# Kernel optimization log

Hardware: AMD Instinct MI355X
Metric: run time of the kernel (lower is better)

Reference implementation:

```python
import jax, jax.numpy as jnp
import numpy as np

C_IN = 96          # spectral bands
D2 = 2 * C_IN      # d = 192 (inner dim)
D4 = 4 * D2        # 768 (4-directional scan channels)
N = 16             # SSM state size
DR = 6             # delta_rank = ceil(96/16)
B, H, W = 2, 96, 96  # H,W not in {8,16,32,64} -> s=1 path


def setup_inputs() -> dict:
    key = jax.random.key(0)
    ks = jax.random.split(key, 8)
    g = lambda k, shape, s: jax.random.normal(k, shape, jnp.float32) * s
    return {
        "x": jax.random.normal(ks[0], (B, C_IN, H, W), jnp.float32),
        "W_in": g(ks[1], (C_IN, 2 * D2), 0.05),          # in_proj (in,out)
        "b_in": jnp.zeros((2 * D2,), jnp.float32),
        "w_dw": g(ks[2], (D2, 1, 3, 3), 0.1),            # depthwise conv OIHW
        "b_dw": jnp.zeros((D2,), jnp.float32),
        "A_log": jnp.log(jnp.tile(jnp.arange(1.0, N + 1.0, dtype=jnp.float32), (D4, 1))),
        "Dp": jnp.ones((D4,), jnp.float32),
        "W_x": g(ks[3], (D4, DR + 2 * N), 0.05),         # x_proj, no bias
        "W_delta": g(ks[4], (DR, D4), 0.1),
        "b_delta": g(ks[5], (D4,), 0.1),
        "ln_g": jnp.ones((D2,), jnp.float32),
        "ln_b": jnp.zeros((D2,), jnp.float32),
        "W_out": g(ks[6], (D2, C_IN), 0.05),             # out_proj, no bias
    }


def _selective_scan(u, delta, A, Bm, Cm, Dv):
    # u, delta: [b,L,d4]; Bm, Cm: [b,L,n]; A: [d4,n]; Dv: [d4]
    b, L, d4 = u.shape
    n = A.shape[1]

    def step(h, inps):
        u_t, dt, B_t, C_t = inps                      # [b,d4],[b,d4],[b,n],[b,n]
        dA = jnp.exp(dt[:, :, None] * A)              # [b,d4,n]
        h = dA * h + (dt * u_t)[:, :, None] * B_t[:, None, :]
        y = jnp.einsum('bdn,bn->bd', h, C_t) + Dv * u_t
        return h, y

    h0 = jnp.zeros((b, d4, n), u.dtype)
    xs = (jnp.swapaxes(u, 0, 1), jnp.swapaxes(delta, 0, 1),
          jnp.swapaxes(Bm, 0, 1), jnp.swapaxes(Cm, 0, 1))
    _, ys = jax.lax.scan(step, h0, xs)                # ys: [L,b,d4]
    return jnp.swapaxes(ys, 0, 1)                     # [b,L,d4]


def reference(x, W_in, b_in, w_dw, b_dw, A_log, Dp, W_x, W_delta, b_delta, ln_g, ln_b, W_out):
    b, c, Hh, Ww = x.shape                            # s = 1 (H not in {8,16,32,64})
    d = W_in.shape[1] // 2
    # in_proj on channel-last, chunk into x / gate z
    xz = jnp.einsum('bchw,ce->bhwe', x, W_in) + b_in  # [b,h,w,2d]
    xx, z = jnp.split(xz, 2, axis=-1)
    # depthwise conv + silu
    xc = jnp.transpose(xx, (0, 3, 1, 2))              # [b,d,h,w]
    xc = jax.lax.conv_general_dilated(
        xc, w_dw, (1, 1), 'SAME', feature_group_count=d,
        dimension_numbers=('NCHW', 'OIHW', 'NCHW')) + b_dw[None, :, None, None]
    xc = jax.nn.silu(xc)
    # 4 directional flattenings (with s=1: x1==x2 row-major, x3==x4 reversed)
    L = Hh * Ww
    flat = xc.reshape(b, d, L)
    flipped = xc[:, :, ::-1, ::-1].reshape(b, d, L)
    xl = jnp.swapaxes(jnp.concatenate([flat, flat, flipped, flipped], axis=1), 1, 2)  # [b,L,4d]
    # SSM parameterization
    A = -jnp.exp(A_log)                               # [4d,n]
    x_dbl = xl @ W_x                                  # [b,L,dr+2n]
    dr, n = W_delta.shape[0], A.shape[1]
    dt_r = x_dbl[..., :dr]
    Bm = x_dbl[..., dr:dr + n]
    Cm = x_dbl[..., dr + n:]
    delta = jax.nn.softplus(dt_r @ W_delta + b_delta)  # [b,L,4d]
    y = _selective_scan(xl, delta, A, Bm, Cm, Dp)      # [b,L,4d]
    # merge 4 directions back to spatial
    y = jnp.transpose(y.reshape(b, L, 4, d), (0, 2, 3, 1))  # [b,4,d,L]
    y1 = y[:, 0].reshape(b, d, Hh, Ww)
    y2 = y[:, 1].reshape(b, d, Hh, Ww)
    y3 = y[:, 2].reshape(b, d, Hh, Ww)[:, :, ::-1, ::-1]
    y4 = y[:, 3].reshape(b, d, Hh, Ww)[:, :, ::-1, ::-1]
    yh = jnp.transpose(y1 + y2 + y3 + y4, (0, 2, 3, 1))  # [b,h,w,d]
    # LayerNorm over d
    mu = yh.mean(-1, keepdims=True)
    var = ((yh - mu) ** 2).mean(-1, keepdims=True)
    yn = (yh - mu) * jax.lax.rsqrt(var + 1e-5) * ln_g + ln_b
    out = (yn * jax.nn.silu(z)) @ W_out               # [b,h,w,c]
    return jnp.transpose(out, (0, 3, 1, 2))           # [b,c,h,w]
```

## Files before the change

kernel.cpp:

```cpp
#include <hip/hip_runtime.h>
#include <hip/hip_bf16.h>
#include <math.h>

#define CIN 96
#define D2 192
#define D4 768
#define LL 9216
#define NN 16
#define NCH 288
#define CLEN 32

typedef float v2f __attribute__((ext_vector_type(2)));

#define SZ_Y4SLOT (2u*2u*9216u*192u)
#define SZ_BL    (2u*9216u*192u)
#define SZ_XDBL  (2u*9216u*38u)
#define SZ_S     (2u*4u*288u*192u)
#define SZ_HSLOT (2u*4u*288u*192u*8u)
#define F_Y4     0u
#define F_XX     0u
#define F_ZS     (F_Y4 + SZ_Y4SLOT)
#define F_XT     (F_ZS + SZ_BL)
#define F_XD0    (F_XT + SZ_BL)
#define F_XD1    (F_XD0 + SZ_XDBL)
#define F_XD2    (F_XD1 + SZ_XDBL)
#define F_XD3    (F_XD2 + SZ_XDBL)
#define F_SBUF   (F_XD3 + SZ_XDBL)
#define F_HBUF   (F_SBUF + SZ_S)
#define F_WCOMB  (F_HBUF + SZ_HSLOT)
#define F_A0     (F_WCOMB + 15360u)
#define F_FF     (F_A0 + 768u)

__device__ __forceinline__ float silu_f(float z) {
    return z / (1.0f + __expf(-z));
}

__global__ __launch_bounds__(256) void k0_foldw(
    const float* __restrict__ Wx, const float* __restrict__ Alog,
    float* __restrict__ wcomb, float* __restrict__ A0f, float* __restrict__ Ffl)
{
    int i = blockIdx.x * 256 + threadIdx.x;
    if (i < 768) {
        float a0 = -__expf(Alog[i * 16]);
        bool fast = true;
        for (int n = 1; n < 16; n++) {
            float an = -__expf(Alog[i * 16 + n]);
            float tgt = (n + 1) * a0;
            fast = fast && (fabsf(an - tgt) <= 1e-5f * fabsf(tgt));
        }
        A0f[i] = a0;
        Ffl[i] = fast ? 1.f : 0.f;
    }
    if (i >= 192 * 80) return;
    int d = i / 80, j = i % 80;
    float v = 0.f;
    if (j < 38) v = Wx[d * 38 + j] + Wx[(d + 192) * 38 + j];
    else if (j >= 40 && j < 78) {
        int jj = j - 40;
        v = Wx[(d + 384) * 38 + jj] + Wx[(d + 576) * 38 + jj];
    }
    wcomb[i] = v;
}

__global__ __launch_bounds__(256) void k1_inproj(
    const float* __restrict__ x, const float* __restrict__ Win,
    const float* __restrict__ bin, float* __restrict__ xx, float* __restrict__ zs)
{
    __shared__ float xs[96][36];
    __shared__ float wsh[96][68];
    int tid = threadIdx.x;
    int bid = blockIdx.x;
    int eh = bid & 1;
    int lt = bid >> 1;
    int gl0 = lt * 32;
    int b = gl0 / LL;
    int l0 = gl0 % LL;

    for (int i = tid; i < 96 * 32; i += 256) {
        int k = i >> 5, li = i & 31;
        xs[k][li] = x[(size_t)(b * 96 + k) * LL + l0 + li];
    }
    int lg = tid & 15;
    int eg = tid >> 4;
    for (int ch = 0; ch < 3; ch++) {
        int ecol0 = eh * 192 + ch * 64;
        __syncthreads();
        for (int i = tid; i < 96 * 64; i += 256) {
            int k = i >> 6, e = i & 63;
            wsh[k][e] = Win[k * 384 + ecol0 + e];
        }
        __syncthreads();
        v2f acc[4];
#pragma unroll
        for (int j = 0; j < 4; j++) { acc[j].x = 0.f; acc[j].y = 0.f; }
        for (int k = 0; k < 96; k++) {
            v2f x2 = *(const v2f*)&xs[k][lg * 2];
            float4 wv = *(const float4*)&wsh[k][eg * 4];
            float wa[4] = {wv.x, wv.y, wv.z, wv.w};
#pragma unroll
            for (int j = 0; j < 4; j++) {
                v2f wsp; wsp.x = wa[j]; wsp.y = wa[j];
                acc[j] += x2 * wsp;
            }
        }
        if (eh == 0) {
#pragma unroll
            for (int j = 0; j < 4; j++) {
                int e = ecol0 + eg * 4 + j;
                float bb = bin[e];
                float2 v = {acc[j].x + bb, acc[j].y + bb};
                *(float2*)&xx[(size_t)(b * 192 + e) * LL + l0 + lg * 2] = v;
            }
        } else {
            int rel0 = ch * 64 + eg * 4;
            float bb0 = bin[ecol0 + eg * 4 + 0];
            float bb1 = bin[ecol0 + eg * 4 + 1];
            float bb2 = bin[ecol0 + eg * 4 + 2];
            float bb3 = bin[ecol0 + eg * 4 + 3];
#pragma unroll
            for (int r = 0; r < 2; r++) {
                int l = l0 + lg * 2 + r;
                float4 v;
                v.x = silu_f(acc[0][r] + bb0);
                v.y = silu_f(acc[1][r] + bb1);
                v.z = silu_f(acc[2][r] + bb2);
                v.w = silu_f(acc[3][r] + bb3);
                *(float4*)&zs[((size_t)b * LL + l) * 192 + rel0] = v;
            }
        }
    }
}

__global__ __launch_bounds__(192) void k2_conv(
    const float* __restrict__ xx, const float* __restrict__ wdw,
    const float* __restrict__ bdw, float* __restrict__ xt)
{
    __shared__ float tile[32][97];
    __shared__ float wsm[32][9];
    __shared__ float bs[32];
    int tid = threadIdx.x;
    int bid = blockIdx.x;
    int h = bid % 96;
    int r = bid / 96;
    int dg = r % 6;
    int b = r / 6;

    for (int i = tid; i < 288; i += 192) wsm[i / 9][i % 9] = wdw[(dg * 32 + i / 9) * 9 + (i % 9)];
    if (tid < 32) bs[tid] = bdw[dg * 32 + tid];
    __syncthreads();

    int w = tid % 96;
    int dhalf = tid / 96;
    for (int p = 0; p < 16; p++) {
        int dsub = 2 * p + dhalf;
        const float* base = xx + (size_t)(b * 192 + dg * 32 + dsub) * LL;
        float acc = bs[dsub];
#pragma unroll
        for (int kh = 0; kh < 3; kh++) {
            int hh = h + kh - 1;
            if (hh < 0 || hh >= 96) continue;
            const float* row = base + hh * 96;
#pragma unroll
            for (int kw = 0; kw < 3; kw++) {
                int ww = w + kw - 1;
                if (ww < 0 || ww >= 96) continue;
                acc += row[ww] * wsm[dsub][kh * 3 + kw];
            }
        }
        tile[dsub][w] = silu_f(acc);
    }
    __syncthreads();
    for (int i = tid; i < 768; i += 192) {
        int q = i & 7, ls = i >> 3;
        float4 v = {tile[q * 4 + 0][ls], tile[q * 4 + 1][ls], tile[q * 4 + 2][ls], tile[q * 4 + 3][ls]};
        *(float4*)&xt[((size_t)b * LL + h * 96 + ls) * 192 + dg * 32 + q * 4] = v;
    }
}

__global__ __launch_bounds__(320) void k3_xdbl(
    const float* __restrict__ xt, const float* __restrict__ wcomb,
    float* __restrict__ xa0, float* __restrict__ xa1,
    float* __restrict__ xb0, float* __restrict__ xb1)
{
    __shared__ float xs[16][68];
    __shared__ float wsh[16][80];
    int tid = threadIdx.x;
    int bid = blockIdx.x;
    int kh = bid & 1;
    int rt = (bid >> 1) % 144;
    int b = bid / 288;
    int r0 = rt * 64;
    int k0 = kh * 96;
    float* __restrict__ xa = kh ? xa1 : xa0;
    float* __restrict__ xb = kh ? xb1 : xb0;

    int rg = tid / 20;
    int cg = tid % 20;
    v2f acc[4][2];
#pragma unroll
    for (int i = 0; i < 4; i++)
#pragma unroll
        for (int p = 0; p < 2; p++) { acc[i][p].x = 0.f; acc[i][p].y = 0.f; }

    for (int kc = 0; kc < 96; kc += 16) {
        __syncthreads();
        if (tid < 256) {
            int row = tid >> 2, dq = tid & 3;
            float4 v = *(const float4*)&xt[((size_t)b * LL + r0 + row) * 192 + k0 + kc + dq * 4];
            xs[dq * 4 + 0][row] = v.x;
            xs[dq * 4 + 1][row] = v.y;
            xs[dq * 4 + 2][row] = v.z;
            xs[dq * 4 + 3][row] = v.w;
        }
        for (int i = tid; i < 16 * 80; i += 320) {
            int d = i / 80, j = i - d * 80;
            wsh[d][j] = wcomb[(k0 + kc + d) * 80 + j];
        }
        __syncthreads();
#pragma unroll
        for (int d = 0; d < 16; d++) {
            float4 xv = *(const float4*)&xs[d][rg * 4];
            float4 wv = *(const float4*)&wsh[d][cg * 4];
            v2f w01; w01.x = wv.x; w01.y = wv.y;
            v2f w23; w23.x = wv.z; w23.y = wv.w;
            float xr[4] = {xv.x, xv.y, xv.z, xv.w};
#pragma unroll
            for (int i = 0; i < 4; i++) {
                v2f xi; xi.x = xr[i]; xi.y = xr[i];
                acc[i][0] += xi * w01;
                acc[i][1] += xi * w23;
            }
        }
    }
    int c0 = cg * 4;
#pragma unroll
    for (int i = 0; i < 4; i++) {
        int la = r0 + rg * 4 + i;
#pragma unroll
        for (int j = 0; j < 4; j++) {
            int col = c0 + j;
            float v = acc[i][j >> 1][j & 1];
            if (col < 38) {
                xa[((size_t)b * LL + la) * 38 + col] = v;
            } else if (col >= 40 && col < 78) {
                int lb = LL - 1 - la;
                xb[((size_t)b * LL + lb) * 38 + (col - 40)] = v;
            }
        }
    }
}

__global__ __launch_bounds__(192, 4) void k4_pass1(
    const float* __restrict__ xt,
    const float* __restrict__ xa0, const float* __restrict__ xa1,
    const float* __restrict__ xb0, const float* __restrict__ xb1,
    const float* __restrict__ Wd, const float* __restrict__ bdl,
    const float* __restrict__ Alog, const float* __restrict__ A0f,
    const float* __restrict__ Ffl,
    float* __restrict__ Sbuf, __hip_bfloat16* __restrict__ Hbuf)
{
    __shared__ float Bt[CLEN][16];
    __shared__ float Dt[CLEN][6];
    int tid = threadIdx.x;
    int bid = blockIdx.x;
    int k = bid % NCH;
    int r = bid / NCH;
    int dir = r & 3;
    int b = r >> 2;
    int l0 = k * CLEN;
    for (int i = tid; i < CLEN * 16; i += 192) {
        int t = i >> 4, n = i & 15;
        size_t rb = ((size_t)b * LL + l0 + t) * 38 + 6 + n;
        Bt[t][n] = (xa0[rb] + xa1[rb]) + (xb0[rb] + xb1[rb]);
    }
    for (int i = tid; i < CLEN * 6; i += 192) {
        int t = i / 6, rr = i - 6 * t;
        size_t rb = ((size_t)b * LL + l0 + t) * 38 + rr;
        Dt[t][rr] = (xa0[rb] + xa1[rb]) + (xb0[rb] + xb1[rb]);
    }
    __syncthreads();
    int c = tid;
    int d4 = dir * 192 + c;
    float a0 = A0f[d4];
    bool fast = (Ffl[d4] != 0.f);
    float wd[6];
#pragma unroll
    for (int rr = 0; rr < 6; rr++) wd[rr] = Wd[rr * 768 + d4];
    float bde = bdl[d4];
    float S = 0.f;
    const float* xtp = xt + (size_t)b * LL * 192 + c;
    int bd = b * 4 + dir;
    size_t base = (((size_t)bd * NCH + k) * 192 + c) * 16;
    if (fast) {
        v2f h2[8];
#pragma unroll
        for (int n = 0; n < 8; n++) { h2[n].x = 0.f; h2[n].y = 0.f; }
#pragma unroll 2
        for (int t = 0; t < CLEN; t++) {
            float2 d01 = *(const float2*)&Dt[t][0];
            float2 d23 = *(const float2*)&Dt[t][2];
            float2 d45 = *(const float2*)&Dt[t][4];
            float s = bde + d01.x * wd[0] + d01.y * wd[1] + d23.x * wd[2]
                          + d23.y * wd[3] + d45.x * wd[4] + d45.y * wd[5];
            float dt = (s > 20.f) ? s : __logf(1.f + __expf(s));
            S += dt;
            int lp = (dir < 2) ? (l0 + t) : (LL - 1 - (l0 + t));
            float u = xtp[(size_t)lp * 192];
            float du = dt * u;
            float e1 = __expf(dt * a0);
            float e2 = e1 * e1;
            v2f q; q.x = e1; q.y = e2;
            v2f e2v; e2v.x = e2; e2v.y = e2;
            v2f e4v = e2v * e2v;
            v2f q2 = q * e2v;
            v2f du2; du2.x = du; du2.y = du;
#pragma unroll
            for (int g = 0; g < 4; g++) {
                float4 bq = *(const float4*)&Bt[t][4 * g];
                v2f b0; b0.x = bq.x; b0.y = bq.y;
                v2f b1; b1.x = bq.z; b1.y = bq.w;
                h2[2 * g]     = q  * h2[2 * g]     + du2 * b0;
                h2[2 * g + 1] = q2 * h2[2 * g + 1] + du2 * b1;
                if (g < 3) { q *= e4v; q2 *= e4v; }
            }
        }
        __hip_bfloat16* hb = Hbuf + base;
#pragma unroll
        for (int n = 0; n < 8; n++) {
            hb[2 * n]     = __float2bfloat16(h2[n].x);
            hb[2 * n + 1] = __float2bfloat16(h2[n].y);
        }
    } else {
        float h[16];
#pragma unroll
        for (int n = 0; n < 16; n++) h[n] = 0.f;
        for (int t = 0; t < CLEN; t++) {
            float s = bde;
#pragma unroll
            for (int rr = 0; rr < 6; rr++) s += Dt[t][rr] * wd[rr];
            float dt = (s > 20.f) ? s : __logf(1.f + __expf(s));
            S += dt;
            int lp = (dir < 2) ? (l0 + t) : (LL - 1 - (l0 + t));
            float u = xtp[(size_t)lp * 192];
            float du = dt * u;
#pragma unroll
            for (int n = 0; n < 16; n++) {
                float e = __expf(dt * (-__expf(Alog[d4 * 16 + n])));
                h[n] = e * h[n] + du * Bt[t][n];
            }
        }
#pragma unroll
        for (int n = 0; n < 16; n++) Hbuf[base + n] = __float2bfloat16(h[n]);
    }
    Sbuf[((size_t)bd * NCH + k) * 192 + c] = S;
}

__global__ __launch_bounds__(256) void k4_pass2(
    const float* __restrict__ Sbuf, const float* __restrict__ Alog,
    __hip_bfloat16* __restrict__ Hbuf)
{
    int lane = blockIdx.x * 256 + threadIdx.x;
    int bd = lane / 3072;
    int cn = lane % 3072;
    int c = cn >> 4, n = cn & 15;
    int dir = bd & 3;
    float an = -__expf(Alog[(dir * 192 + c) * 16 + n]);
    float h = 0.f;
#pragma unroll 8
    for (int k = 0; k < NCH; k++) {
        size_t sidx = ((size_t)bd * NCH + k) * 192 + c;
        float S = Sbuf[sidx];
        size_t idx = sidx * 16 + n;
        float hl = __bfloat162float(Hbuf[idx]);
        float P = __expf(an * S);
        Hbuf[idx] = __float2bfloat16(h);
        h = P * h + hl;
    }
}

__global__ __launch_bounds__(192, 4) void k4_pass3(
    const float* __restrict__ xt,
    const float* __restrict__ xa0, const float* __restrict__ xa1,
    const float* __restrict__ xb0, const float* __restrict__ xb1,
    const float* __restrict__ Wd, const float* __restrict__ bdl,
    const float* __restrict__ Alog, const float* __restrict__ A0f,
    const float* __restrict__ Ffl, const float* __restrict__ Dp,
    const __hip_bfloat16* __restrict__ Hbuf, __hip_bfloat16* __restrict__ y4)
{
    __shared__ float Bt[CLEN][16];
    __shared__ float Ct[CLEN][16];
    __shared__ float Dt[CLEN][6];
    int tid = threadIdx.x;
    int bid = blockIdx.x;
    int k = bid % NCH;
    int r = bid / NCH;
    int dir = r & 3;
    int b = r >> 2;
    int l0 = k * CLEN;
    for (int i = tid; i < CLEN * 16; i += 192) {
        int t = i >> 4, n = i & 15;
        size_t rb = ((size_t)b * LL + l0 + t) * 38;
        size_t r1 = rb + 6 + n, r2 = rb + 22 + n;
        Bt[t][n] = (xa0[r1] + xa1[r1]) + (xb0[r1] + xb1[r1]);
        Ct[t][n] = (xa0[r2] + xa1[r2]) + (xb0[r2] + xb1[r2]);
    }
    for (int i = tid; i < CLEN * 6; i += 192) {
        int t = i / 6, rr = i - 6 * t;
        size_t rb = ((size_t)b * LL + l0 + t) * 38 + rr;
        Dt[t][rr] = (xa0[rb] + xa1[rb]) + (xb0[rb] + xb1[rb]);
    }
    __syncthreads();
    int c = tid;
    int d4 = dir * 192 + c;
    float a0 = A0f[d4];
    bool fast = (Ffl[d4] != 0.f);
    float wd[6];
#pragma unroll
    for (int rr = 0; rr < 6; rr++) wd[rr] = Wd[rr * 768 + d4];
    float bde = bdl[d4];
    float Dv = Dp[d4];
    int bd = b * 4 + dir;
    size_t base = (((size_t)bd * NCH + k) * 192 + c) * 16;
    const float* xtp = xt + (size_t)b * LL * 192 + c;
    __hip_bfloat16* yp = y4 + (size_t)bd * LL * 192 + c;
    if (fast) {
        v2f h2[8];
        const __hip_bfloat16* hb = Hbuf + base;
#pragma unroll
        for (int n = 0; n < 8; n++) {
            h2[n].x = __bfloat162float(hb[2 * n]);
            h2[n].y = __bfloat162float(hb[2 * n + 1]);
        }
#pragma unroll 2
        for (int t = 0; t < CLEN; t++) {
            float2 d01 = *(const float2*)&Dt[t][0];
            float2 d23 = *(const float2*)&Dt[t][2];
            float2 d45 = *(const float2*)&Dt[t][4];
            float s = bde + d01.x * wd[0] + d01.y * wd[1] + d23.x * wd[2]
                          + d23.y * wd[3] + d45.x * wd[4] + d45.y * wd[5];
            float dt = (s > 20.f) ? s : __logf(1.f + __expf(s));
            int lp = (dir < 2) ? (l0 + t) : (LL - 1 - (l0 + t));
            float u = xtp[(size_t)lp * 192];
            float du = dt * u;
            float e1 = __expf(dt * a0);
            float e2 = e1 * e1;
            v2f q; q.x = e1; q.y = e2;
            v2f e2v; e2v.x = e2; e2v.y = e2;
            v2f e4v = e2v * e2v;
            v2f q2 = q * e2v;
            v2f du2; du2.x = du; du2.y = du;
            v2f ya; ya.x = 0.f; ya.y = 0.f;
            v2f yb; yb.x = 0.f; yb.y = 0.f;
#pragma unroll
            for (int g = 0; g < 4; g++) {
                float4 bq = *(const float4*)&Bt[t][4 * g];
                float4 cq = *(const float4*)&Ct[t][4 * g];
                v2f b0; b0.x = bq.x; b0.y = bq.y;
                v2f b1; b1.x = bq.z; b1.y = bq.w;
                v2f c0v; c0v.x = cq.x; c0v.y = cq.y;
                v2f c1v; c1v.x = cq.z; c1v.y = cq.w;
                h2[2 * g]     = q  * h2[2 * g]     + du2 * b0;
                ya += h2[2 * g] * c0v;
                h2[2 * g + 1] = q2 * h2[2 * g + 1] + du2 * b1;
                yb += h2[2 * g + 1] * c1v;
                if (g < 3) { q *= e4v; q2 *= e4v; }
            }
            float yv = (ya.x + ya.y) + (yb.x + yb.y) + Dv * u;
            yp[(size_t)lp * 192] = __float2bfloat16(yv);
        }
    } else {
        float h[16];
#pragma unroll
        for (int n = 0; n < 16; n++) h[n] = __bfloat162float(Hbuf[base + n]);
        for (int t = 0; t < CLEN; t++) {
            float s = bde;
#pragma unroll
            for (int rr = 0; rr < 6; rr++) s += Dt[t][rr] * wd[rr];
            float dt = (s > 20.f) ? s : __logf(1.f + __expf(s));
            int lp = (dir < 2) ? (l0 + t) : (LL - 1 - (l0 + t));
            float u = xtp[(size_t)lp * 192];
            float du = dt * u;
            float yv = Dv * u;
#pragma unroll
            for (int n = 0; n < 16; n++) {
                float e = __expf(dt * (-__expf(Alog[d4 * 16 + n])));
                h[n] = e * h[n] + du * Bt[t][n];
                yv += h[n] * Ct[t][n];
            }
            yp[(size_t)lp * 192] = __float2bfloat16(yv);
        }
    }
}

__global__ __launch_bounds__(256) void k5_out(
    const __hip_bfloat16* __restrict__ y4, const float* __restrict__ zs,
    const float* __restrict__ lng, const float* __restrict__ lnb,
    const float* __restrict__ Wout, float* __restrict__ out)
{
    __shared__ float acts[16][196];
    __shared__ float wsh[32][100];
    int tid = threadIdx.x;
    int wv = tid >> 6;
    int lane = tid & 63;
    int gl0 = blockIdx.x * 16;
    int b = gl0 / LL;
    int l0 = gl0 % LL;
    const size_t ds = (size_t)LL * 192;

    for (int i = 0; i < 4; i++) {
        int rrow = wv * 4 + i;
        int l = l0 + rrow;
        float yv[3], zv[3];
        float s1 = 0.f, s2 = 0.f;
#pragma unroll
        for (int kk = 0; kk < 3; kk++) {
            int c = lane + kk * 64;
            size_t off = ((size_t)(b * 4) * LL + l) * 192 + c;
            float y = __bfloat162float(y4[off]) + __bfloat162float(y4[off + ds])
                    + __bfloat162float(y4[off + 2 * ds]) + __bfloat162float(y4[off + 3 * ds]);
            yv[kk] = y;
            zv[kk] = zs[((size_t)b * LL + l) * 192 + c];
            s1 += y; s2 += y * y;
        }
#pragma unroll
        for (int o = 32; o; o >>= 1) {
            s1 += __shfl_xor(s1, o, 64);
            s2 += __shfl_xor(s2, o, 64);
        }
        float mean = s1 * (1.f / 192.f);
        float var = s2 * (1.f / 192.f) - mean * mean;
        float rs = rsqrtf(var + 1e-5f);
#pragma unroll
        for (int kk = 0; kk < 3; kk++) {
            int c = lane + kk * 64;
            float yn = (yv[kk] - mean) * rs * lng[c] + lnb[c];
            acts[rrow][c] = yn * zv[kk];
        }
    }

    int ty = tid & 15;
    int tx = tid >> 4;
    v2f o2[3];
    o2[0].x = 0.f; o2[0].y = 0.f;
    o2[1].x = 0.f; o2[1].y = 0.f;
    o2[2].x = 0.f; o2[2].y = 0.f;

    for (int kc = 0; kc < 192; kc += 32) {
        __syncthreads();
        for (int i = tid; i < 32 * 24; i += 256) {
            int d = i / 24, q = i - d * 24;
            *(float4*)&wsh[d][q * 4] = *(const float4*)&Wout[(kc + d) * 96 + q * 4];
        }
        __syncthreads();
#pragma unroll
        for (int kk = 0; kk < 32; kk++) {
            float av = acts[ty][kc + kk];
            const v2f* wp = (const v2f*)&wsh[kk][tx * 6];
            v2f w0 = wp[0], w1 = wp[1], w2 = wp[2];
            v2f sp; sp.x = av; sp.y = av;
            o2[0] += sp * w0;
            o2[1] += sp * w1;
            o2[2] += sp * w2;
        }
    }
    int l = l0 + ty;
#pragma unroll
    for (int j = 0; j < 6; j++) {
        int n = tx * 6 + j;
        out[((size_t)(b * 96) + n) * LL + l] = o2[j >> 1][j & 1];
    }
}

extern "C" void kernel_launch(void* const* d_in, const int* in_sizes, int n_in,
                              void* d_out, int out_size, void* d_ws, size_t ws_size,
                              hipStream_t stream)
{
    const float* x    = (const float*)d_in[0];
    const float* Win  = (const float*)d_in[1];
    const float* bin  = (const float*)d_in[2];
    const float* wdw  = (const float*)d_in[3];
    const float* bdw  = (const float*)d_in[4];
    const float* Alog = (const float*)d_in[5];
    const float* Dp   = (const float*)d_in[6];
    const float* Wx   = (const float*)d_in[7];
    const float* Wd   = (const float*)d_in[8];
    const float* bdl  = (const float*)d_in[9];
    const float* lng  = (const float*)d_in[10];
    const float* lnb  = (const float*)d_in[11];
    const float* Wout = (const float*)d_in[12];
    float* out = (float*)d_out;

    float* ws    = (float*)d_ws;
    __hip_bfloat16* y4 = (__hip_bfloat16*)(ws + F_Y4);
    float* xx    = ws + F_XX;
    float* zs    = ws + F_ZS;
    float* xt    = ws + F_XT;
    float* xd0   = ws + F_XD0;
    float* xd1   = ws + F_XD1;
    float* xd2   = ws + F_XD2;
    float* xd3   = ws + F_XD3;
    float* Sbuf  = ws + F_SBUF;
    __hip_bfloat16* Hbuf = (__hip_bfloat16*)(ws + F_HBUF);
    float* wcomb = ws + F_WCOMB;
    float* A0f   = ws + F_A0;
    float* Ffl   = ws + F_FF;

    k0_foldw<<<60, 256, 0, stream>>>(Wx, Alog, wcomb, A0f, Ffl);
    k1_inproj<<<1152, 256, 0, stream>>>(x, Win, bin, xx, zs);
    k2_conv<<<1152, 192, 0, stream>>>(xx, wdw, bdw, xt);
    k3_xdbl<<<576, 320, 0, stream>>>(xt, wcomb, xd0, xd1, xd2, xd3);
    k4_pass1<<<2304, 192, 0, stream>>>(xt, xd0, xd1, xd2, xd3, Wd, bdl, Alog, A0f, Ffl, Sbuf, Hbuf);
    k4_pass2<<<96, 256, 0, stream>>>(Sbuf, Alog, Hbuf);
    k4_pass3<<<2304, 192, 0, stream>>>(xt, xd0, xd1, xd2, xd3, Wd, bdl, Alog, A0f, Ffl, Dp, Hbuf, y4);
    k5_out<<<1152, 256, 0, stream>>>(y4, zs, lng, lnb, Wout, out);
}
```

Baseline: 294.1 us.

## Retile in_proj GEMM to 64x96 tiles with K-chunked staging; relax scan occupancy hints

The in_proj kernel now computes a 64-position by 96-column tile per block, loads x and W_in in 32-deep K chunks with float4 loads, and gives each thread a 4x6 register tile instead of 2x4. Each shared-memory value is reused more per load and global traffic per output drops, at the cost of more registers per thread. The grid mapping changes to match, so the host launch count must be 4*144*2 blocks. The two scan-pass kernels also swap launch_bounds min-blocks for an amdgpu_waves_per_eu(2,4) hint, which gives the compiler more register room.

Result: no change. 293.3 us (-0.3%).

```diff
diff --git a/kernel.cpp b/kernel.cpp
--- a/kernel.cpp
+++ b/kernel.cpp
@@ -66,66 +66,76 @@
     const float* __restrict__ x, const float* __restrict__ Win,
     const float* __restrict__ bin, float* __restrict__ xx, float* __restrict__ zs)
 {
-    __shared__ float xs[96][36];
-    __shared__ float wsh[96][68];
+    __shared__ float xs[32][68];
+    __shared__ float wsh[32][100];
     int tid = threadIdx.x;
     int bid = blockIdx.x;
-    int eh = bid & 1;
-    int lt = bid >> 1;
-    int gl0 = lt * 32;
-    int b = gl0 / LL;
-    int l0 = gl0 % LL;
-
-    for (int i = tid; i < 96 * 32; i += 256) {
-        int k = i >> 5, li = i & 31;
-        xs[k][li] = x[(size_t)(b * 96 + k) * LL + l0 + li];
-    }
+    int eq = bid & 3;
+    int lt = (bid >> 2) % 144;
+    int b = bid / 576;
+    int l0 = lt * 64;
+    int e0 = eq * 96;
+
     int lg = tid & 15;
-    int eg = tid >> 4;
-    for (int ch = 0; ch < 3; ch++) {
-        int ecol0 = eh * 192 + ch * 64;
+    int cg = tid >> 4;
+    v2f acc[4][3];
+#pragma unroll
+    for (int i = 0; i < 4; i++)
+#pragma unroll
+        for (int p = 0; p < 3; p++) { acc[i][p].x = 0.f; acc[i][p].y = 0.f; }
+
+    for (int kc = 0; kc < 96; kc += 32) {
         __syncthreads();
-        for (int i = tid; i < 96 * 64; i += 256) {
-            int k = i >> 6, e = i & 63;
-            wsh[k][e] = Win[k * 384 + ecol0 + e];
+        for (int i = tid; i < 512; i += 256) {
+            int kk = i >> 4, q = i & 15;
+            float4 v = *(const float4*)&x[(size_t)(b * 96 + kc + kk) * LL + l0 + q * 4];
+            *(float4*)&xs[kk][q * 4] = v;
+        }
+        for (int i = tid; i < 768; i += 256) {
+            int kk = i / 24, q = i - kk * 24;
+            float4 v = *(const float4*)&Win[(kc + kk) * 384 + e0 + q * 4];
+            *(float4*)&wsh[kk][q * 4] = v;
         }
         __syncthreads();
-        v2f acc[4];
-#pragma unroll
-        for (int j = 0; j < 4; j++) { acc[j].x = 0.f; acc[j].y = 0.f; }
-        for (int k = 0; k < 96; k++) {
-            v2f x2 = *(const v2f*)&xs[k][lg * 2];
-            float4 wv = *(const float4*)&wsh[k][eg * 4];
-            float wa[4] = {wv.x, wv.y, wv.z, wv.w};
-#pragma unroll
-            for (int j = 0; j < 4; j++) {
-                v2f wsp; wsp.x = wa[j]; wsp.y = wa[j];
-                acc[j] += x2 * wsp;
-            }
-        }
-        if (eh == 0) {
-#pragma unroll
-            for (int j = 0; j < 4; j++) {
-                int e = ecol0 + eg * 4 + j;
-                float bb = bin[e];
-                float2 v = {acc[j].x + bb, acc[j].y + bb};
-                *(float2*)&xx[(size_t)(b * 192 + e) * LL + l0 + lg * 2] = v;
-            }
-        } else {
-            int rel0 = ch * 64 + eg * 4;
-            float bb0 = bin[ecol0 + eg * 4 + 0];
-            float bb1 = bin[ecol0 + eg * 4 + 1];
-            float bb2 = bin[ecol0 + eg * 4 + 2];
-            float bb3 = bin[ecol0 + eg * 4 + 3];
-#pragma unroll
-            for (int r = 0; r < 2; r++) {
-                int l = l0 + lg * 2 + r;
-                float4 v;
-                v.x = silu_f(acc[0][r] + bb0);
-                v.y = silu_f(acc[1][r] + bb1);
-                v.z = silu_f(acc[2][r] + bb2);
-                v.w = silu_f(acc[3][r] + bb3);
-                *(float4*)&zs[((size_t)b * LL + l) * 192 + rel0] = v;
+#pragma unroll 4
+        for (int k = 0; k < 32; k++) {
+            float4 xv = *(const float4*)&xs[k][lg * 4];
+            const v2f* wp = (const v2f*)&wsh[k][cg * 6];
+            v2f w0 = wp[0], w1 = wp[1], w2 = wp[2];
+            float xa[4] = {xv.x, xv.y, xv.z, xv.w};
+#pragma unroll
+            for (int i = 0; i < 4; i++) {
+                v2f xi; xi.x = xa[i]; xi.y = xa[i];
+                acc[i][0] += xi * w0;
+                acc[i][1] += xi * w1;
+                acc[i][2] += xi * w2;
+            }
+        }
+    }
+    if (eq < 2) {
+#pragma unroll
+        for (int j = 0; j < 6; j++) {
+            int e = e0 + cg * 6 + j;
+            float bb = bin[e];
+            float4 v = {acc[0][j >> 1][j & 1] + bb, acc[1][j >> 1][j & 1] + bb,
+                        acc[2][j >> 1][j & 1] + bb, acc[3][j >> 1][j & 1] + bb};
+            *(float4*)&xx[(size_t)(b * 192 + e) * LL + l0 + lg * 4] = v;
+        }
+    } else {
+        int zc0 = e0 - 192 + cg * 6;
+        float bb[6];
+#pragma unroll
+        for (int j = 0; j < 6; j++) bb[j] = bin[e0 + cg * 6 + j];
+#pragma unroll
+        for (int i = 0; i < 4; i++) {
+            int l = l0 + lg * 4 + i;
+            float* zp = &zs[((size_t)b * LL + l) * 192 + zc0];
+#pragma unroll
+            for (int p = 0; p < 3; p++) {
+                float2 v;
+                v.x = silu_f(acc[i][p].x + bb[2 * p]);
+                v.y = silu_f(acc[i][p].y + bb[2 * p + 1]);
+                *(float2*)&zp[2 * p] = v;
             }
         }
     }
@@ -250,7 +260,7 @@
     }
 }
 
-__global__ __launch_bounds__(192, 4) void k4_pass1(
+__global__ __launch_bounds__(192) __attribute__((amdgpu_waves_per_eu(2, 4))) void k4_pass1(
     const float* __restrict__ xt,
     const float* __restrict__ xa0, const float* __restrict__ xa1,
     const float* __restrict__ xb0, const float* __restrict__ xb1,
@@ -378,7 +388,7 @@
     }
 }
 
-__global__ __launch_bounds__(192, 4) void k4_pass3(
+__global__ __launch_bounds__(192) __attribute__((amdgpu_waves_per_eu(2, 4))) void k4_pass3(
     const float* __restrict__ xt,
     const float* __restrict__ xa0, const float* __restrict__ xa1,
     const float* __restrict__ xb0, const float* __restrict__ xb1,
```
